# Kernel optimization log

Hardware: AMD Instinct MI355X
Metric: run time of the kernel (lower is better)

Reference implementation:

```python
import jax, jax.numpy as jnp
import numpy as np

N, E, H, G = 50000, 500000, 64, 64


def _ln(x, g, b):
    m = jnp.mean(x, -1, keepdims=True)
    v = jnp.var(x, -1, keepdims=True)
    return (x - m) * jax.lax.rsqrt(v + 1e-5) * g + b


def _mlp_ln(x, w1, b1, w2, b2, g, be):
    # Linear -> ReLU -> (Dropout eval no-op) -> Linear -> LayerNorm
    h = jax.nn.relu(x @ w1 + b1)
    return _ln(h @ w2 + b2, g, be)


def setup_inputs() -> dict:
    key = jax.random.key(0)
    ks = jax.random.split(key, 24)
    w = lambda i, s: jax.random.normal(ks[i], s, dtype=jnp.float32) * 0.1
    z = lambda s: jnp.zeros(s, jnp.float32)
    o = lambda s: jnp.ones(s, jnp.float32)
    inp = {
        'x': jax.random.normal(ks[0], (N, 3), dtype=jnp.float32),
        'edge_index': jax.random.randint(ks[1], (2, E), 0, N),
        'edge_attr': jax.random.normal(ks[2], (E, 3), dtype=jnp.float32),
        'batch': jnp.sort(jax.random.randint(ks[3], (N,), 0, G)),
        'ne_w1': w(4, (3, H)), 'ne_b1': z((H,)), 'ne_w2': w(5, (H, H)), 'ne_b2': z((H,)), 'ne_g': o((H,)), 'ne_be': z((H,)),
        'ee_w1': w(6, (3, H)), 'ee_b1': z((H,)), 'ee_w2': w(7, (H, H)), 'ee_b2': z((H,)), 'ee_g': o((H,)), 'ee_be': z((H,)),
        'gin0_eps': z((1,)), 'gin0_w1': w(8, (H, H)), 'gin0_b1': z((H,)), 'gin0_w2': w(9, (H, H)), 'gin0_b2': z((H,)), 'gin0_g': o((H,)), 'gin0_be': z((H,)),
        'gin1_eps': z((1,)), 'gin1_w1': w(10, (H, H)), 'gin1_b1': z((H,)), 'gin1_w2': w(11, (H, H)), 'gin1_b2': z((H,)), 'gin1_g': o((H,)), 'gin1_be': z((H,)),
        'gp_w': w(12, (H, H)), 'gp_b': z((H,)), 'gp_g': o((H,)), 'gp_be': z((H,)),
        'ep_w1': w(13, (4 * H, 2 * H)), 'ep_b1': z((2 * H,)),
        'ep_w2': w(14, (2 * H, H)), 'ep_b2': z((H,)),
        'ep_w3': w(15, (H, 1)), 'ep_b3': z((1,)),
    }
    return inp


def reference(x, edge_index, edge_attr, batch,
              ne_w1, ne_b1, ne_w2, ne_b2, ne_g, ne_be,
              ee_w1, ee_b1, ee_w2, ee_b2, ee_g, ee_be,
              gin0_eps, gin0_w1, gin0_b1, gin0_w2, gin0_b2, gin0_g, gin0_be,
              gin1_eps, gin1_w1, gin1_b1, gin1_w2, gin1_b2, gin1_g, gin1_be,
              gp_w, gp_b, gp_g, gp_be,
              ep_w1, ep_b1, ep_w2, ep_b2, ep_w3, ep_b3):
    src, dst = edge_index[0], edge_index[1]
    # encoders
    h = _mlp_ln(x, ne_w1, ne_b1, ne_w2, ne_b2, ne_g, ne_be)            # [N, H]
    ef = _mlp_ln(edge_attr, ee_w1, ee_b1, ee_w2, ee_b2, ee_g, ee_be)   # [E, H]
    # GINEConv layer 0: mlp((1+eps)*x + scatter_add(relu(x_src + e)))
    msg = jax.nn.relu(h[src] + ef)
    aggr = jnp.zeros_like(h).at[dst].add(msg)
    h = _mlp_ln((1.0 + gin0_eps) * h + aggr, gin0_w1, gin0_b1, gin0_w2, gin0_b2, gin0_g, gin0_be)
    h = jax.nn.relu(h)  # inter-layer activation (dropout eval no-op)
    # GINEConv layer 1
    msg = jax.nn.relu(h[src] + ef)
    aggr = jnp.zeros_like(h).at[dst].add(msg)
    h = _mlp_ln((1.0 + gin1_eps) * h + aggr, gin1_w1, gin1_b1, gin1_w2, gin1_b2, gin1_g, gin1_be)
    # global mean pool over graphs
    seg = jax.ops.segment_sum(h, batch, num_segments=G)                            # [G, H]
    cnt = jax.ops.segment_sum(jnp.ones((h.shape[0], 1), h.dtype), batch, num_segments=G)
    gp = seg / jnp.maximum(cnt, 1.0)
    gf = _ln(jax.nn.relu(gp @ gp_w + gp_b), gp_g, gp_be)                           # [G, H]
    # edge predictor on [src | dst | global | edge] = [E, 4H]
    c = jnp.concatenate([h[src], h[dst], gf[batch[src]], ef], axis=-1)
    t = jnp.tanh(c @ ep_w1 + ep_b1)
    t = jnp.tanh(t @ ep_w2 + ep_b2)
    return jax.nn.sigmoid(t @ ep_w3 + ep_b3)  # [E, 1]
```

## Files before the change

### kernel.cpp

```cpp
#include <hip/hip_runtime.h>
#include <hip/hip_bf16.h>

typedef unsigned int uint;
typedef unsigned short ushort;
typedef __attribute__((ext_vector_type(8))) short short8;
typedef __attribute__((ext_vector_type(4))) float floatx4;

__device__ __forceinline__ float bf2f(ushort u) { return __uint_as_float(((uint)u) << 16); }
__device__ __forceinline__ ushort f2bf(float f) {
  uint u = __float_as_uint(f);
  u += 0x7fffu + ((u >> 16) & 1u);
  return (ushort)(u >> 16);
}
__device__ __forceinline__ uint pk2(float a, float b) {
  return (uint)f2bf(a) | ((uint)f2bf(b) << 16);
}
__device__ __forceinline__ float ldf(const void* p, long i, int m) {
  if (m) return bf2f(((const ushort*)p)[i]);
  return ((const float*)p)[i];
}
__device__ __forceinline__ int get_md(const uint* mdp) {
  return (mdp[0] == 0x3F800000u) ? 0 : 1;
}
__device__ __forceinline__ float fast_rcp(float x) { return __builtin_amdgcn_rcpf(x); }
__device__ __forceinline__ float tanh_fast(float x) {
  float e = __builtin_amdgcn_exp2f(2.8853900818f * x);
  return fmaf(-2.f, fast_rcp(1.f + e), 1.f);
}
__device__ __forceinline__ float sigmoid_fast(float x) {
  float e = __builtin_amdgcn_exp2f(-1.4426950409f * x);
  return fast_rcp(1.f + e);
}
__device__ __forceinline__ void gll16(const void* g, void* l) {
  __builtin_amdgcn_global_load_lds(
      (const __attribute__((address_space(1))) uint*)g,
      (__attribute__((address_space(3))) uint*)l, 16, 0, 0);
}

__global__ __launch_bounds__(256) void k_enc_mfma(
    const void* __restrict__ in, int R,
    const void* __restrict__ w1, const void* __restrict__ b1,
    const ushort* __restrict__ w2sw_, const void* __restrict__ b2,
    const void* __restrict__ gam, const void* __restrict__ bet,
    ushort* __restrict__ outp, ushort* __restrict__ outp2,
    const int* __restrict__ epos, const uint* __restrict__ mdp)
{
  __shared__ float xs[64*3];
  __shared__ float w1s[192], b1s[64], b2s[64], gs[64], bs2[64];
  __shared__ __align__(16) ushort T_s[64 * 72];
  int md = get_md(mdp);
  int tid = threadIdx.x;
  long e0 = (long)blockIdx.x * 64;
  if (tid < 192) {
    w1s[tid] = ldf(w1, tid, md);
    int row = tid / 3, cc = tid - row*3;
    long e = e0 + row;
    xs[tid] = (e < R) ? ldf(in, e*3 + cc, md) : 0.f;
  }
  if (tid < 64) { b1s[tid] = ldf(b1, tid, md); b2s[tid] = ldf(b2, tid, md);
                  gs[tid] = ldf(gam, tid, md); bs2[tid] = ldf(bet, tid, md); }
  __syncthreads();
  int lane = tid & 63, wv = tid >> 6;
  int quad = lane >> 4, mm = lane & 15;
  float x0 = xs[(wv*16 + mm)*3 + 0];
  float x1 = xs[(wv*16 + mm)*3 + 1];
  float x2 = xs[(wv*16 + mm)*3 + 2];
  short8 af[2];
#pragma unroll
  for (int s = 0; s < 2; ++s) {
#pragma unroll
    for (int j = 0; j < 8; ++j) {
      int f = s*32 + quad*8 + j;
      float hv = fmaxf(b1s[f] + x0*w1s[f] + x1*w1s[64+f] + x2*w1s[128+f], 0.f);
      af[s][j] = (short)f2bf(hv);
    }
  }
  floatx4 acc[4] = {};
  const short8* Bp = (const short8*)w2sw_;
#pragma unroll
  for (int s = 0; s < 2; ++s) {
#pragma unroll
    for (int t = 0; t < 4; ++t) {
      short8 b = Bp[(s*4 + t)*64 + lane];
      acc[t] = __builtin_amdgcn_mfma_f32_16x16x32_bf16(af[s], b, acc[t], 0, 0, 0);
    }
  }
  float vv[4][4];
#pragma unroll
  for (int t = 0; t < 4; ++t) {
    float bb = b2s[mm + 16*t];
#pragma unroll
    for (int r = 0; r < 4; ++r) vv[t][r] = acc[t][r] + bb;
  }
  float mr[4], vr[4];
#pragma unroll
  for (int r = 0; r < 4; ++r) {
    float s = vv[0][r] + vv[1][r] + vv[2][r] + vv[3][r];
#pragma unroll
    for (int off = 1; off < 16; off <<= 1) s += __shfl_xor(s, off);
    mr[r] = s * 0.015625f;
    float q = 0.f;
#pragma unroll
    for (int t = 0; t < 4; ++t) { float d = vv[t][r] - mr[r]; q = fmaf(d, d, q); }
#pragma unroll
    for (int off = 1; off < 16; off <<= 1) q += __shfl_xor(q, off);
    vr[r] = rsqrtf(q * 0.015625f + 1e-5f);
  }
#pragma unroll
  for (int t = 0; t < 4; ++t) {
    int col = mm + 16*t;
    float g = gs[col], be = bs2[col];
#pragma unroll
    for (int r = 0; r < 4; ++r)
      T_s[(wv*16 + quad*4 + r)*72 + col] = f2bf((vv[t][r] - mr[r]) * vr[r] * g + be);
  }
  __syncthreads();
#pragma unroll
  for (int i = 0; i < 2; ++i) {
    int gi = tid + 256*i;
    int row = gi >> 3, c = gi & 7;
    long e = e0 + row;
    if (e < R) {
      uint4 v = *(const uint4*)&T_s[row*72 + c*8];
      ((uint4*)(outp + e*64))[c] = v;
      if (outp2)
        ((uint4*)(outp2 + (long)epos[e]*64))[c] = v;
    }
  }
}

__global__ __launch_bounds__(256) void k_swz(
    const void* __restrict__ w1, const void* __restrict__ w2,
    const void* __restrict__ w2e, const void* __restrict__ w2n,
    const void* __restrict__ gw10, const void* __restrict__ gw20,
    const void* __restrict__ gw11, const void* __restrict__ gw21,
    ushort* __restrict__ w1sw, ushort* __restrict__ w2sw,
    ushort* __restrict__ ew2sw, ushort* __restrict__ nw2sw,
    ushort* __restrict__ g0w1sw, ushort* __restrict__ g0w2sw,
    ushort* __restrict__ g1w1sw, ushort* __restrict__ g1w2sw,
    int* __restrict__ deg, float* __restrict__ gsum, int Nn,
    const uint* __restrict__ mdp)
{
  int md = get_md(mdp);
  int i = blockIdx.x * 256 + threadIdx.x;
  int nthr = gridDim.x * 256;
  for (int k = i; k < Nn; k += nthr) deg[k] = 0;
  for (int k = i; k < 64*64 + 64; k += nthr) gsum[k] = 0.f;
  if (i < 32768) {
    int q = i & 7, lane = (i >> 3) & 63, tt = (i >> 9) & 7, s = i >> 12;
    int k = s*32 + (lane >> 4)*8 + q, n = (lane & 15) + 16*tt;
    w1sw[i] = f2bf(ldf(w1, k*128 + n, md));
  }
  if (i < 8192) {
    int q = i & 7, lane = (i >> 3) & 63, tt = (i >> 9) & 3, s = i >> 11;
    int k = s*32 + (lane >> 4)*8 + q, n = (lane & 15) + 16*tt;
    int src = k*64 + n;
    w2sw[i]   = f2bf(ldf(w2,   src, md));
    ew2sw[i]  = f2bf(ldf(w2e,  src, md));
    nw2sw[i]  = f2bf(ldf(w2n,  src, md));
    g0w1sw[i] = f2bf(ldf(gw10, src, md));
    g0w2sw[i] = f2bf(ldf(gw20, src, md));
    g1w1sw[i] = f2bf(ldf(gw11, src, md));
    g1w2sw[i] = f2bf(ldf(gw21, src, md));
  }
}

__global__ __launch_bounds__(256) void k_deg(
    const int* __restrict__ ei, int* __restrict__ deg, int E_)
{
  int e = blockIdx.x * 256 + threadIdx.x;
  if (e < E_) atomicAdd(&deg[ei[E_ + e]], 1);
}

__global__ __launch_bounds__(256) void k_scan1(
    const int* __restrict__ deg, int* __restrict__ rs, int* __restrict__ bsum, int Nn)
{
  __shared__ int ls[256];
  int tid = threadIdx.x;
  int i = blockIdx.x * 256 + tid;
  int v = (i < Nn) ? deg[i] : 0;
  ls[tid] = v;
  __syncthreads();
  for (int off = 1; off < 256; off <<= 1) {
    int t = (tid >= off) ? ls[tid - off] : 0;
    __syncthreads();
    ls[tid] += t;
    __syncthreads();
  }
  if (i < Nn) rs[i] = ls[tid] - v;
  if (tid == 255) bsum[blockIdx.x] = ls[255];
}

__global__ __launch_bounds__(256) void k_scan2(
    int* __restrict__ bsum, int nb, int* __restrict__ rs, int Nn)
{
  __shared__ int ls[256];
  int tid = threadIdx.x;
  int chunk = (nb + 255) / 256;
  int c0 = tid * chunk, c1 = min(c0 + chunk, nb);
  int sum = 0;
  for (int i = c0; i < c1; ++i) sum += bsum[i];
  ls[tid] = sum;
  __syncthreads();
  for (int off = 1; off < 256; off <<= 1) {
    int t = (tid >= off) ? ls[tid - off] : 0;
    __syncthreads();
    ls[tid] += t;
    __syncthreads();
  }
  int run = ls[tid] - sum;
  for (int i = c0; i < c1; ++i) { int d = bsum[i]; bsum[i] = run; run += d; }
  if (tid == 255) rs[Nn] = ls[255];
}

__global__ __launch_bounds__(256) void k_scan3(
    int* __restrict__ rs, int* __restrict__ cur,
    const int* __restrict__ bsum, int Nn)
{
  int i = blockIdx.x * 256 + threadIdx.x;
  if (i < Nn) {
    int v = rs[i] + bsum[blockIdx.x];
    rs[i] = v;
    cur[i] = v;
  }
}

__global__ __launch_bounds__(256) void k_fill(
    const int* __restrict__ ei, int* __restrict__ cur,
    int2* __restrict__ ep, int* __restrict__ epos, int E_)
{
  int e = blockIdx.x * 256 + threadIdx.x;
  if (e < E_) {
    int s = ei[e];
    int d = ei[E_ + e];
    int p = atomicAdd(&cur[d], 1);
    ep[p] = make_int2(e, s);
    epos[e] = p;
  }
}

__global__ __launch_bounds__(256) void k_aggr(
    const ushort* __restrict__ hbu, const ushort* __restrict__ efp,
    const int2* __restrict__ ep, const int* __restrict__ rs,
    float* __restrict__ aggr, int Nn)
{
  int gw = (blockIdx.x * 256 + threadIdx.x) >> 6;
  int j = threadIdx.x & 63;
  if (gw >= Nn) return;
  int s0 = rs[gw], s1 = rs[gw + 1];
  float acc = 0.f;
  int idx = s0;
  for (; idx + 2 <= s1; idx += 2) {
    int2 a = ep[idx];
    int2 b = ep[idx + 1];
    float fA = bf2f(efp[(long)idx*64 + j]);
    float fB = bf2f(efp[(long)(idx+1)*64 + j]);
    float hA = bf2f(hbu[(long)a.y*64 + j]);
    float hB = bf2f(hbu[(long)b.y*64 + j]);
    acc += fmaxf(hA + fA, 0.f) + fmaxf(hB + fB, 0.f);
  }
  if (idx < s1) {
    int2 a = ep[idx];
    acc += fmaxf(bf2f(hbu[(long)a.y*64 + j]) + bf2f(efp[(long)idx*64 + j]), 0.f);
  }
  aggr[(long)gw*64 + j] = acc;
}

__global__ __launch_bounds__(256) void k_gine_mfma(
    const ushort* __restrict__ hbin, const float* __restrict__ aggr, int Nn,
    const void* __restrict__ epsp,
    const ushort* __restrict__ w1sw_, const void* __restrict__ b1,
    const ushort* __restrict__ w2sw_, const void* __restrict__ b2,
    const void* __restrict__ gam, const void* __restrict__ bet,
    ushort* __restrict__ hbout, int post_relu, const uint* __restrict__ mdp)
{
  __shared__ __align__(16) ushort Ws1[4096], Ws2[4096];
  __shared__ __align__(16) ushort T_s[64 * 72];
  __shared__ float b1s[64], b2s[64], gs[64], bs2[64];
  int md = get_md(mdp);
  int tid = threadIdx.x;
  {
    const uint4* p1 = (const uint4*)w1sw_;
    const uint4* p2 = (const uint4*)w2sw_;
    ((uint4*)Ws1)[tid] = p1[tid];
    ((uint4*)Ws1)[tid + 256] = p1[tid + 256];
    ((uint4*)Ws2)[tid] = p2[tid];
    ((uint4*)Ws2)[tid + 256] = p2[tid + 256];
  }
  if (tid < 64) { b1s[tid] = ldf(b1, tid, md); b2s[tid] = ldf(b2, tid, md);
                  gs[tid] = ldf(gam, tid, md); bs2[tid] = ldf(bet, tid, md); }
  float ope = 1.f + ldf(epsp, 0, md);
  int lane = tid & 63, wv = tid >> 6;
  int quad = lane >> 4, mm = lane & 15;
  long node = (long)blockIdx.x * 64 + wv*16 + mm;
  long nc = (node < Nn) ? node : (long)(Nn - 1);
  const ushort* hrow = hbin + nc*64;
  const float*  arow = aggr + nc*64;
  short8 af[2];
#pragma unroll
  for (int s = 0; s < 2; ++s) {
    int c = s*4 + quad;
    short8 hv = *(const short8*)(hrow + c*8);
    float4 a0 = *(const float4*)(arow + c*8);
    float4 a1 = *(const float4*)(arow + c*8 + 4);
    float uu[8];
    uu[0] = fmaf(bf2f((ushort)hv[0]), ope, a0.x);
    uu[1] = fmaf(bf2f((ushort)hv[1]), ope, a0.y);
    uu[2] = fmaf(bf2f((ushort)hv[2]), ope, a0.z);
    uu[3] = fmaf(bf2f((ushort)hv[3]), ope, a0.w);
    uu[4] = fmaf(bf2f((ushort)hv[4]), ope, a1.x);
    uu[5] = fmaf(bf2f((ushort)hv[5]), ope, a1.y);
    uu[6] = fmaf(bf2f((ushort)hv[6]), ope, a1.z);
    uu[7] = fmaf(bf2f((ushort)hv[7]), ope, a1.w);
#pragma unroll
    for (int j = 0; j < 8; ++j) af[s][j] = (short)f2bf(uu[j]);
  }
  __syncthreads();
  floatx4 acc[4] = {};
#pragma unroll
  for (int s = 0; s < 2; ++s) {
#pragma unroll
    for (int t = 0; t < 4; ++t) {
      short8 b = *(const short8*)&Ws1[((s*4 + t)*64 + lane)*8];
      acc[t] = __builtin_amdgcn_mfma_f32_16x16x32_bf16(af[s], b, acc[t], 0, 0, 0);
    }
  }
#pragma unroll
  for (int t = 0; t < 4; ++t) {
    int col = mm + 16*t;
    float bb = b1s[col];
#pragma unroll
    for (int r = 0; r < 4; ++r)
      T_s[(wv*16 + quad*4 + r)*72 + col] = f2bf(fmaxf(acc[t][r] + bb, 0.f));
  }
  __syncthreads();
  short8 af2[2];
#pragma unroll
  for (int s = 0; s < 2; ++s)
    af2[s] = *(const short8*)&T_s[(wv*16 + mm)*72 + s*32 + quad*8];
  floatx4 acc2[4] = {};
#pragma unroll
  for (int s = 0; s < 2; ++s) {
#pragma unroll
    for (int t = 0; t < 4; ++t) {
      short8 b = *(const short8*)&Ws2[((s*4 + t)*64 + lane)*8];
      acc2[t] = __builtin_amdgcn_mfma_f32_16x16x32_bf16(af2[s], b, acc2[t], 0, 0, 0);
    }
  }
  float vv[4][4];
#pragma unroll
  for (int t = 0; t < 4; ++t) {
    float bb = b2s[mm + 16*t];
#pragma unroll
    for (int r = 0; r < 4; ++r) vv[t][r] = acc2[t][r] + bb;
  }
  float mr[4], vr[4];
#pragma unroll
  for (int r = 0; r < 4; ++r) {
    float s = vv[0][r] + vv[1][r] + vv[2][r] + vv[3][r];
#pragma unroll
    for (int off = 1; off < 16; off <<= 1) s += __shfl_xor(s, off);
    mr[r] = s * 0.015625f;
    float q = 0.f;
#pragma unroll
    for (int t = 0; t < 4; ++t) { float d = vv[t][r] - mr[r]; q = fmaf(d, d, q); }
#pragma unroll
    for (int off = 1; off < 16; off <<= 1) q += __shfl_xor(q, off);
    vr[r] = rsqrtf(q * 0.015625f + 1e-5f);
  }
  __syncthreads();
#pragma unroll
  for (int t = 0; t < 4; ++t) {
    int col = mm + 16*t;
    float g = gs[col], be = bs2[col];
#pragma unroll
    for (int r = 0; r < 4; ++r) {
      float o = (vv[t][r] - mr[r]) * vr[r] * g + be;
      if (post_relu) o = fmaxf(o, 0.f);
      T_s[(wv*16 + quad*4 + r)*72 + col] = f2bf(o);
    }
  }
  __syncthreads();
#pragma unroll
  for (int i = 0; i < 2; ++i) {
    int gi = tid + 256*i;
    int row = gi >> 3, c = gi & 7;
    long n2 = (long)blockIdx.x * 64 + row;
    if (n2 < Nn)
      ((uint4*)(hbout + n2*64))[c] = *(const uint4*)&T_s[row*72 + c*8];
  }
}

__global__ __launch_bounds__(256) void k_pool_f(
    const ushort* __restrict__ hbu, const int* __restrict__ batch,
    float* __restrict__ gsum, float* __restrict__ gcnt, int Nn)
{
  int gw = (blockIdx.x * 256 + threadIdx.x) >> 6;
  int j = threadIdx.x & 63;
  long r0 = (long)gw * 64;
  if (r0 >= Nn) return;
  long rend = min(r0 + 64, (long)Nn);
  float acc = 0.f; int cur = batch[r0]; int run = 0;
  for (long r = r0; r < rend; ++r) {
    int g = batch[r];
    if (g != cur) {
      atomicAdd(&gsum[cur*64 + j], acc);
      if (j == 0) atomicAdd(&gcnt[cur], (float)run);
      acc = 0.f; run = 0; cur = g;
    }
    acc += bf2f(hbu[r*64 + j]);
    run++;
  }
  atomicAdd(&gsum[cur*64 + j], acc);
  if (j == 0) atomicAdd(&gcnt[cur], (float)run);
}

__global__ __launch_bounds__(64) void k_pool_fin_f(
    const float* __restrict__ gsum, const float* __restrict__ gcnt,
    const void* __restrict__ gpw, const void* __restrict__ gpb,
    const void* __restrict__ gpg, const void* __restrict__ gpbe,
    ushort* __restrict__ gfb, const uint* __restrict__ mdp)
{
  __shared__ float wgs[4096];
  __shared__ float us[64];
  int md = get_md(mdp);
  int j = threadIdx.x;
  int g = blockIdx.x;
  for (int i = j; i < 4096; i += 64) wgs[i] = ldf(gpw, i, md);
  float ic = 1.f / fmaxf(gcnt[g], 1.f);
  us[j] = gsum[g*64 + j] * ic;
  __syncthreads();
  float t = ldf(gpb, j, md);
#pragma unroll
  for (int k = 0; k < 64; ++k) t = fmaf(us[k], wgs[k*64 + j], t);
  t = fmaxf(t, 0.f);
  float m = t;
#pragma unroll
  for (int off = 1; off < 64; off <<= 1) m += __shfl_xor(m, off);
  m *= 0.015625f;
  float d = t - m;
  float v = d * d;
#pragma unroll
  for (int off = 1; off < 64; off <<= 1) v += __shfl_xor(v, off);
  float rs = rsqrtf(v * 0.015625f + 1e-5f);
  gfb[g*64 + j] = f2bf(d * rs * ldf(gpg, j, md) + ldf(gpbe, j, md));
}

__global__ __launch_bounds__(256, 4) void k_pred_mfma(
    const ushort* __restrict__ hb, const ushort* __restrict__ efu,
    const ushort* __restrict__ gfb, const int* __restrict__ ei,
    const int* __restrict__ batch,
    const ushort* __restrict__ w1sw, const ushort* __restrict__ w2sw,
    const void* __restrict__ pb1, const void* __restrict__ pb2,
    const void* __restrict__ pw3, const void* __restrict__ pb3,
    void* __restrict__ out, int E_, const uint* __restrict__ mdp)
{
  __shared__ __align__(16) ushort Ws[8192];
  __shared__ __align__(16) ushort T_s[64 * 136];
  __shared__ float b1s[128], b2s[64], w3s[64];
  int md = get_md(mdp);
  int tid = threadIdx.x;
  if (tid < 128) b1s[tid] = ldf(pb1, tid, md);
  if (tid < 64) { b2s[tid] = ldf(pb2, tid, md); w3s[tid] = ldf(pw3, tid, md); }
  long e0 = (long)blockIdx.x * 128;
  int lane = tid & 63, wv = tid >> 6;
  int quad = lane >> 4, mm = lane & 15;
  long eA = e0 + wv*16 + mm;       if (eA >= E_) eA = E_ - 1;
  long eB = e0 + 64 + wv*16 + mm;  if (eB >= E_) eB = E_ - 1;
  int siA = ei[eA], diA = ei[E_ + eA];
  int siB = ei[eB], diB = ei[E_ + eB];
  int giA = batch[siA], giB = batch[siB];
  char* wsb = (char*)Ws + wv*1024;
  int sgo = wv*1024 + lane*16;
  floatx4 acc[16] = {};
#pragma unroll
  for (int q = 0; q < 4; ++q) {
    const ushort* bp; uint oA, oB;
    if (q == 0)      { bp = hb;  oA = (uint)siA * 128u; oB = (uint)siB * 128u; }
    else if (q == 1) { bp = hb;  oA = (uint)diA * 128u; oB = (uint)diB * 128u; }
    else if (q == 2) { bp = gfb; oA = (uint)giA * 128u; oB = (uint)giB * 128u; }
    else             { bp = efu; oA = (uint)eA  * 128u; oB = (uint)eB  * 128u; }
    __syncthreads();
    {
      const char* wq = (const char*)w1sw + q*16384 + sgo;
#pragma unroll
      for (int i = 0; i < 4; ++i)
        gll16(wq + i*4096, wsb + i*4096);
    }
    short8 aA0 = *(const short8*)((const char*)bp + oA + quad*16);
    short8 aA1 = *(const short8*)((const char*)bp + oA + 64 + quad*16);
    short8 aB0 = *(const short8*)((const char*)bp + oB + quad*16);
    short8 aB1 = *(const short8*)((const char*)bp + oB + 64 + quad*16);
    __syncthreads();
#pragma unroll
    for (int t = 0; t < 8; ++t) {
      short8 b = *(const short8*)&Ws[(t*64 + lane)*8];
      acc[t]   = __builtin_amdgcn_mfma_f32_16x16x32_bf16(aA0, b, acc[t],   0, 0, 0);
      acc[8+t] = __builtin_amdgcn_mfma_f32_16x16x32_bf16(aB0, b, acc[8+t], 0, 0, 0);
    }
#pragma unroll
    for (int t = 0; t < 8; ++t) {
      short8 b = *(const short8*)&Ws[((8 + t)*64 + lane)*8];
      acc[t]   = __builtin_amdgcn_mfma_f32_16x16x32_bf16(aA1, b, acc[t],   0, 0, 0);
      acc[8+t] = __builtin_amdgcn_mfma_f32_16x16x32_bf16(aB1, b, acc[8+t], 0, 0, 0);
    }
  }
#pragma unroll
  for (int t = 0; t < 8; ++t) {
    float bb = b1s[mm + 16*t];
#pragma unroll
    for (int r = 0; r < 4; ++r)
      T_s[(16*wv + quad*4 + r)*136 + mm + 16*t] = f2bf(tanh_fast(acc[t][r] + bb));
  }
  __syncthreads();
  {
    const char* wq2 = (const char*)w2sw + sgo;
#pragma unroll
    for (int i = 0; i < 4; ++i)
      gll16(wq2 + i*4096, wsb + i*4096);
  }
  __syncthreads();
  float b3 = ldf(pb3, 0, md);
#pragma unroll
  for (int g = 0; g < 2; ++g) {
    if (g) {
#pragma unroll
      for (int t = 0; t < 8; ++t) {
        float bb = b1s[mm + 16*t];
#pragma unroll
        for (int r = 0; r < 4; ++r)
          T_s[(16*wv + quad*4 + r)*136 + mm + 16*t] = f2bf(tanh_fast(acc[8+t][r] + bb));
      }
    }
    floatx4 acc2[4] = {};
#pragma unroll
    for (int s2 = 0; s2 < 4; ++s2) {
      short8 a = *(const short8*)&T_s[(16*wv + mm)*136 + s2*32 + quad*8];
#pragma unroll
      for (int t = 0; t < 4; ++t) {
        short8 b = *(const short8*)&Ws[((s2*4 + t)*64 + lane)*8];
        acc2[t] = __builtin_amdgcn_mfma_f32_16x16x32_bf16(a, b, acc2[t], 0, 0, 0);
      }
    }
    float p0 = 0.f, p1 = 0.f, p2 = 0.f, p3 = 0.f;
#pragma unroll
    for (int t = 0; t < 4; ++t) {
      int col = mm + 16*t;
      float bb = b2s[col], w3v = w3s[col];
      p0 = fmaf(tanh_fast(acc2[t][0] + bb), w3v, p0);
      p1 = fmaf(tanh_fast(acc2[t][1] + bb), w3v, p1);
      p2 = fmaf(tanh_fast(acc2[t][2] + bb), w3v, p2);
      p3 = fmaf(tanh_fast(acc2[t][3] + bb), w3v, p3);
    }
#pragma unroll
    for (int off = 1; off < 16; off <<= 1) {
      p0 += __shfl_xor(p0, off);
      p1 += __shfl_xor(p1, off);
      p2 += __shfl_xor(p2, off);
      p3 += __shfl_xor(p3, off);
    }
    if (mm == 0) {
      long eb = e0 + g*64 + 16*wv + quad*4;
      float ps[4] = {p0, p1, p2, p3};
#pragma unroll
      for (int r = 0; r < 4; ++r) {
        if (eb + r < E_) {
          float sg = sigmoid_fast(ps[r] + b3);
          if (md) ((ushort*)out)[eb + r] = f2bf(sg);
          else    ((float*)out)[eb + r]  = sg;
        }
      }
    }
  }
}

extern "C" void kernel_launch(void* const* d_in, const int* in_sizes, int n_in,
                              void* d_out, int out_size, void* d_ws, size_t ws_size,
                              hipStream_t stream)
{
  const void* x     = d_in[0];
  const int*  ei    = (const int*)d_in[1];
  const void* eattr = d_in[2];
  const int*  batch = (const int*)d_in[3];
  const void* ne_w1 = d_in[4];  const void* ne_b1 = d_in[5];
  const void* ne_w2 = d_in[6];  const void* ne_b2 = d_in[7];
  const void* ne_g  = d_in[8];  const void* ne_be = d_in[9];
  const void* ee_w1 = d_in[10]; const void* ee_b1 = d_in[11];
  const void* ee_w2 = d_in[12]; const void* ee_b2 = d_in[13];
  const void* ee_g  = d_in[14]; const void* ee_be = d_in[15];
  const void* g0_ep = d_in[16];
  const void* g0_w1 = d_in[17]; const void* g0_b1 = d_in[18];
  const void* g0_w2 = d_in[19]; const void* g0_b2 = d_in[20];
  const void* g0_g  = d_in[21]; const void* g0_be = d_in[22];
  const void* g1_ep = d_in[23];
  const void* g1_w1 = d_in[24]; const void* g1_b1 = d_in[25];
  const void* g1_w2 = d_in[26]; const void* g1_b2 = d_in[27];
  const void* g1_g  = d_in[28]; const void* g1_be = d_in[29];
  const void* gp_w  = d_in[30]; const void* gp_b  = d_in[31];
  const void* gp_g  = d_in[32]; const void* gp_be = d_in[33];
  const void* ep_w1 = d_in[34]; const void* ep_b1 = d_in[35];
  const void* ep_w2 = d_in[36]; const void* ep_b2 = d_in[37];
  const void* ep_w3 = d_in[38]; const void* ep_b3 = d_in[39];

  int N = in_sizes[3];
  int E = in_sizes[1] / 2;
  const uint* mdp = (const uint*)ne_g;

  char* ws = (char*)d_ws;
  size_t off = 0;
  auto alloc = [&](size_t bytes) { char* p = ws + off; off += (bytes + 255) & ~(size_t)255; return p; };
  ushort* hb     = (ushort*)alloc((size_t)N * 64 * 2);
  ushort* efu    = (ushort*)alloc((size_t)E * 64 * 2);
  ushort* efp    = (ushort*)alloc((size_t)E * 64 * 2);
  float*  aggr   = (float*) alloc((size_t)N * 64 * 4);
  float*  gsum   = (float*) alloc((64 * 64 + 64) * 4);
  float*  gcnt   = gsum + 64 * 64;
  ushort* gfb    = (ushort*)alloc(64 * 64 * 2);
  ushort* w1sw   = (ushort*)alloc(32768 * 2);
  ushort* w2sw   = (ushort*)alloc(8192 * 2);
  ushort* ew2sw  = (ushort*)alloc(8192 * 2);
  ushort* nw2sw  = (ushort*)alloc(8192 * 2);
  ushort* g0w1sw = (ushort*)alloc(8192 * 2);
  ushort* g0w2sw = (ushort*)alloc(8192 * 2);
  ushort* g1w1sw = (ushort*)alloc(8192 * 2);
  ushort* g1w2sw = (ushort*)alloc(8192 * 2);
  int*    deg    = (int*)   alloc((size_t)N * 4);
  int*    rs     = (int*)   alloc((size_t)(N + 1) * 4);
  int*    cur    = (int*)   alloc((size_t)N * 4);
  int2*   ep     = (int2*)  alloc((size_t)E * 8);
  int*    epos   = (int*)   alloc((size_t)E * 4);
  int*    bsum   = (int*)   alloc((size_t)((N + 255) / 256) * 4);
  (void)ws_size; (void)n_in; (void)out_size;

  int gN = (N + 255) / 256;
  int gE = (E + 255) / 256;
  int gE64 = (E + 63) / 64;
  int gE128 = (E + 127) / 128;
  int gN64 = (N + 63) / 64;
  int gAggr = (int)(((long)N * 64 + 255) / 256);
  int gPool = ((N + 63) / 64 + 3) / 4;

  k_swz<<<128, 256, 0, stream>>>(ep_w1, ep_w2, ee_w2, ne_w2, g0_w1, g0_w2, g1_w1, g1_w2,
                                 w1sw, w2sw, ew2sw, nw2sw,
                                 g0w1sw, g0w2sw, g1w1sw, g1w2sw,
                                 deg, gsum, N, mdp);
  k_deg<<<gE, 256, 0, stream>>>(ei, deg, E);
  k_scan1<<<gN, 256, 0, stream>>>(deg, rs, bsum, N);
  k_scan2<<<1, 256, 0, stream>>>(bsum, gN, rs, N);
  k_scan3<<<gN, 256, 0, stream>>>(rs, cur, bsum, N);
  k_fill<<<gE, 256, 0, stream>>>(ei, cur, ep, epos, E);
  k_enc_mfma<<<gN64, 256, 0, stream>>>(x, N, ne_w1, ne_b1, nw2sw, ne_b2, ne_g, ne_be,
                                       hb, (ushort*)nullptr, (const int*)nullptr, mdp);
  k_enc_mfma<<<gE64, 256, 0, stream>>>(eattr, E, ee_w1, ee_b1, ew2sw, ee_b2, ee_g, ee_be,
                                       efu, efp, epos, mdp);
  k_aggr<<<gAggr, 256, 0, stream>>>(hb, efp, ep, rs, aggr, N);
  k_gine_mfma<<<gN64, 256, 0, stream>>>(hb, aggr, N, g0_ep, g0w1sw, g0_b1, g0w2sw, g0_b2,
                                        g0_g, g0_be, hb, 1, mdp);
  k_aggr<<<gAggr, 256, 0, stream>>>(hb, efp, ep, rs, aggr, N);
  k_gine_mfma<<<gN64, 256, 0, stream>>>(hb, aggr, N, g1_ep, g1w1sw, g1_b1, g1w2sw, g1_b2,
                                        g1_g, g1_be, hb, 0, mdp);
  k_pool_f<<<gPool, 256, 0, stream>>>(hb, batch, gsum, gcnt, N);
  k_pool_fin_f<<<64, 64, 0, stream>>>(gsum, gcnt, gp_w, gp_b, gp_g, gp_be, gfb, mdp);
  k_pred_mfma<<<gE128, 256, 0, stream>>>(hb, efu, gfb, ei, batch, w1sw, w2sw,
                                         ep_b1, ep_b2, ep_w3, ep_b3, d_out, E, mdp);
}
```

Before: 445.3 us.

## Double-buffer predictor weight slices and prefetch next gather during MFMA

The edge predictor kernel now keeps two LDS weight buffers. It loads the next quarter of W1, or W2 on the last step, and gathers the next feature rows while the current quarter's MFMAs run, which removes one sync per step. The goal is to hide global gather and weight-load latency behind compute. It also drops the occupancy hint from launch_bounds and swaps the manual bf16 rounding for a compiler cast. The cost is doubled LDS (about 32KB for Ws plus T_s) and more live registers, so fewer blocks may fit per CU.

After: 449.4 us. About the same (+0.9%).

```diff
diff --git a/kernel.cpp b/kernel.cpp
--- a/kernel.cpp
+++ b/kernel.cpp
@@ -8,12 +8,10 @@
 
 __device__ __forceinline__ float bf2f(ushort u) { return __uint_as_float(((uint)u) << 16); }
 __device__ __forceinline__ ushort f2bf(float f) {
-  uint u = __float_as_uint(f);
-  u += 0x7fffu + ((u >> 16) & 1u);
-  return (ushort)(u >> 16);
-}
-__device__ __forceinline__ uint pk2(float a, float b) {
-  return (uint)f2bf(a) | ((uint)f2bf(b) << 16);
+  __bf16 h = (__bf16)f;
+  ushort u;
+  __builtin_memcpy(&u, &h, 2);
+  return u;
 }
 __device__ __forceinline__ float ldf(const void* p, long i, int m) {
   if (m) return bf2f(((const ushort*)p)[i]);
@@ -446,7 +444,7 @@
   gfb[g*64 + j] = f2bf(d * rs * ldf(gpg, j, md) + ldf(gpbe, j, md));
 }
 
-__global__ __launch_bounds__(256, 4) void k_pred_mfma(
+__global__ __launch_bounds__(256) void k_pred_mfma(
     const ushort* __restrict__ hb, const ushort* __restrict__ efu,
     const ushort* __restrict__ gfb, const int* __restrict__ ei,
     const int* __restrict__ batch,
@@ -455,7 +453,7 @@
     const void* __restrict__ pw3, const void* __restrict__ pb3,
     void* __restrict__ out, int E_, const uint* __restrict__ mdp)
 {
-  __shared__ __align__(16) ushort Ws[8192];
+  __shared__ __align__(16) ushort Ws[2][8192];
   __shared__ __align__(16) ushort T_s[64 * 136];
   __shared__ float b1s[128], b2s[64], w3s[64];
   int md = get_md(mdp);
@@ -470,39 +468,62 @@
   int siA = ei[eA], diA = ei[E_ + eA];
   int siB = ei[eB], diB = ei[E_ + eB];
   int giA = batch[siA], giB = batch[siB];
-  char* wsb = (char*)Ws + wv*1024;
+  char* wsb0 = (char*)Ws[0] + wv*1024;
+  char* wsb1 = (char*)Ws[1] + wv*1024;
   int sgo = wv*1024 + lane*16;
+
+  auto gather = [&](int qq, short8& A0, short8& A1, short8& B0, short8& B1) {
+    const char* bp; uint oA, oB;
+    if (qq == 0)      { bp = (const char*)hb;  oA = (uint)siA*128u; oB = (uint)siB*128u; }
+    else if (qq == 1) { bp = (const char*)hb;  oA = (uint)diA*128u; oB = (uint)diB*128u; }
+    else if (qq == 2) { bp = (const char*)gfb; oA = (uint)giA*128u; oB = (uint)giB*128u; }
+    else              { bp = (const char*)efu; oA = (uint)eA*128u;  oB = (uint)eB*128u; }
+    A0 = *(const short8*)(bp + oA + quad*16);
+    A1 = *(const short8*)(bp + oA + 64 + quad*16);
+    B0 = *(const short8*)(bp + oB + quad*16);
+    B1 = *(const short8*)(bp + oB + 64 + quad*16);
+  };
+
+  {
+    const char* wq = (const char*)w1sw + sgo;
+#pragma unroll
+    for (int i = 0; i < 4; ++i) gll16(wq + i*4096, wsb0 + i*4096);
+  }
+  short8 cA0, cA1, cB0, cB1;
+  gather(0, cA0, cA1, cB0, cB1);
+  __syncthreads();
+
   floatx4 acc[16] = {};
 #pragma unroll
   for (int q = 0; q < 4; ++q) {
-    const ushort* bp; uint oA, oB;
-    if (q == 0)      { bp = hb;  oA = (uint)siA * 128u; oB = (uint)siB * 128u; }
-    else if (q == 1) { bp = hb;  oA = (uint)diA * 128u; oB = (uint)diB * 128u; }
-    else if (q == 2) { bp = gfb; oA = (uint)giA * 128u; oB = (uint)giB * 128u; }
-    else             { bp = efu; oA = (uint)eA  * 128u; oB = (uint)eB  * 128u; }
-    __syncthreads();
-    {
-      const char* wq = (const char*)w1sw + q*16384 + sgo;
-#pragma unroll
-      for (int i = 0; i < 4; ++i)
-        gll16(wq + i*4096, wsb + i*4096);
-    }
-    short8 aA0 = *(const short8*)((const char*)bp + oA + quad*16);
-    short8 aA1 = *(const short8*)((const char*)bp + oA + 64 + quad*16);
-    short8 aB0 = *(const short8*)((const char*)bp + oB + quad*16);
-    short8 aB1 = *(const short8*)((const char*)bp + oB + 64 + quad*16);
-    __syncthreads();
+    char* dstb = (q & 1) ? wsb0 : wsb1;
+    if (q < 3) {
+      const char* wq = (const char*)w1sw + (q+1)*16384 + sgo;
+#pragma unroll
+      for (int i = 0; i < 4; ++i) gll16(wq + i*4096, dstb + i*4096);
+    } else {
+      const char* wq2 = (const char*)w2sw + sgo;
+#pragma unroll
+      for (int i = 0; i < 4; ++i) gll16(wq2 + i*4096, wsb0 + i*4096);
+    }
+    short8 nA0, nA1, nB0, nB1;
+    if (q < 3) gather(q+1, nA0, nA1, nB0, nB1);
+    const ushort* Bq = Ws[q & 1];
 #pragma unroll
     for (int t = 0; t < 8; ++t) {
-      short8 b = *(const short8*)&Ws[(t*64 + lane)*8];
-      acc[t]   = __builtin_amdgcn_mfma_f32_16x16x32_bf16(aA0, b, acc[t],   0, 0, 0);
-      acc[8+t] = __builtin_amdgcn_mfma_f32_16x16x32_bf16(aB0, b, acc[8+t], 0, 0, 0);
+      short8 b = *(const short8*)&Bq[(t*64 + lane)*8];
+      acc[t]   = __builtin_amdgcn_mfma_f32_16x16x32_bf16(cA0, b, acc[t],   0, 0, 0);
+      acc[8+t] = __builtin_amdgcn_mfma_f32_16x16x32_bf16(cB0, b, acc[8+t], 0, 0, 0);
     }
 #pragma unroll
     for (int t = 0; t < 8; ++t) {
-      short8 b = *(const short8*)&Ws[((8 + t)*64 + lane)*8];
-      acc[t]   = __builtin_amdgcn_mfma_f32_16x16x32_bf16(aA1, b, acc[t],   0, 0, 0);
-      acc[8+t] = __builtin_amdgcn_mfma_f32_16x16x32_bf16(aB1, b, acc[8+t], 0, 0, 0);
+      short8 b = *(const short8*)&Bq[((8 + t)*64 + lane)*8];
+      acc[t]   = __builtin_amdgcn_mfma_f32_16x16x32_bf16(cA1, b, acc[t],   0, 0, 0);
+      acc[8+t] = __builtin_amdgcn_mfma_f32_16x16x32_bf16(cB1, b, acc[8+t], 0, 0, 0);
+    }
+    if (q < 3) {
+      __syncthreads();
+      cA0 = nA0; cA1 = nA1; cB0 = nB0; cB1 = nB1;
     }
   }
 #pragma unroll
@@ -511,13 +532,6 @@
 #pragma unroll
     for (int r = 0; r < 4; ++r)
       T_s[(16*wv + quad*4 + r)*136 + mm + 16*t] = f2bf(tanh_fast(acc[t][r] + bb));
-  }
-  __syncthreads();
-  {
-    const char* wq2 = (const char*)w2sw + sgo;
-#pragma unroll
-    for (int i = 0; i < 4; ++i)
-      gll16(wq2 + i*4096, wsb + i*4096);
   }
   __syncthreads();
   float b3 = ldf(pb3, 0, md);
@@ -538,7 +552,7 @@
       short8 a = *(const short8*)&T_s[(16*wv + mm)*136 + s2*32 + quad*8];
 #pragma unroll
       for (int t = 0; t < 4; ++t) {
-        short8 b = *(const short8*)&Ws[((s2*4 + t)*64 + lane)*8];
+        short8 b = *(const short8*)&Ws[0][((s2*4 + t)*64 + lane)*8];
         acc2[t] = __builtin_amdgcn_mfma_f32_16x16x32_bf16(a, b, acc2[t], 0, 0, 0);
       }
     }
```
